# Optimization experiments

Hardware: AMD Instinct MI355X
Metric: run time of the kernel (lower is better)

The kernel has to match this reference:

```python
import jax, jax.numpy as jnp
import numpy as np

D_MODEL = 2048
D_STATE = 64
D_HEAD = 64
EXPAND = 2
CHUNK = 256
D_INNER = EXPAND * D_MODEL          # 4096
N_HEADS = D_INNER // D_HEAD          # 64
PARAM_DIM = 1 + 2 * D_STATE          # 129


def setup_inputs() -> dict:
    key = jax.random.key(0)
    k0, k1, k2, k3 = jax.random.split(key, 4)
    x = jax.random.normal(k0, (1, 4096, D_MODEL), jnp.float32)
    w_in = jax.random.normal(k1, (2 * D_INNER, D_MODEL), jnp.float32) * 0.02
    w_param = jax.random.normal(k2, (N_HEADS * PARAM_DIM, D_MODEL), jnp.float32) * 0.02
    w_out = jax.random.normal(k3, (D_MODEL, D_INNER), jnp.float32) * 0.02
    return {"x": x, "w_in": w_in, "w_param": w_param, "w_out": w_out}


def _ssd(a, Bm, Cm, X, Q):
    # a: (nb, l), Bm/Cm: (nb, l, ds), X: (nb, l, dh). Mamba-2 SSD chunked scan.
    nb, l = a.shape
    ds = Bm.shape[-1]
    dh = X.shape[-1]
    nc = l // Q
    la = jnp.log(a).reshape(nb, nc, Q)
    cs = jnp.cumsum(la, axis=-1)                      # cumulative log-decay within chunk
    Bc = Bm.reshape(nb, nc, Q, ds)
    Cc = Cm.reshape(nb, nc, Q, ds)
    Xc = X.reshape(nb, nc, Q, dh)
    # intra-chunk (attention-like dual): L[i,j] = prod_{r=j+1..i} a_r, j<=i
    tri = jnp.tril(jnp.ones((Q, Q), bool))
    L = jnp.where(tri, jnp.exp(cs[..., :, None] - cs[..., None, :]), 0.0)
    scores = jnp.einsum('znid,znjd->znij', Cc, Bc) * L
    y_diag = jnp.einsum('znij,znjh->znih', scores, Xc)
    # per-chunk state contribution: sum_j decay_to_end[j] * B_j^T x_j -> (nb,nc,ds,dh)
    decay_states = jnp.exp(cs[..., -1:] - cs)
    states = jnp.einsum('znj,znjd,znjh->zndh', decay_states, Bc, Xc)
    A_chunk = jnp.exp(cs[..., -1])                    # total decay per chunk (nb, nc)
    def step(S, inp):
        Ac, st = inp
        S_prev = S
        return Ac[:, None, None] * S + st, S_prev
    S0 = jnp.zeros((nb, ds, dh), a.dtype)
    _, S_prev = jax.lax.scan(step, S0, (A_chunk.T, jnp.moveaxis(states, 1, 0)))
    S_prev = jnp.moveaxis(S_prev, 0, 1)               # state entering each chunk (nb,nc,ds,dh)
    y_inter = jnp.einsum('znid,zndh,zni->znih', Cc, S_prev, jnp.exp(cs))
    return (y_diag + y_inter).reshape(nb, l, dh)


def reference(x, w_in, w_param, w_out):
    b, l, _ = x.shape
    xr = x @ w_in.T                                   # (b, l, 2*d_inner)
    inp, res = xr[..., :D_INNER], xr[..., D_INNER:]
    params = (x @ w_param.T).reshape(b, l, N_HEADS, PARAM_DIM)
    dt = jax.nn.softplus(params[..., 0])
    a = jnp.exp(-dt)                                  # (b, l, n_heads)
    Bp = params[..., 1:1 + D_STATE]
    Cp = params[..., 1 + D_STATE:]
    nb = b * N_HEADS
    # NOTE: raw row-major reshapes, mirroring the torch source exactly
    y = _ssd(a.reshape(nb, l),
             Bp.reshape(nb, l, D_STATE),
             Cp.reshape(nb, l, D_STATE),
             inp.reshape(nb, l, D_HEAD),
             CHUNK)
    y = y.reshape(b, l, D_INNER)
    out = y * jax.nn.silu(res)
    return out @ w_out.T
```

## Files before the change

### kernel.cpp

```cpp
#include <hip/hip_runtime.h>
#include <math.h>

#define Q 256

typedef unsigned short u16;
typedef unsigned int u32;
typedef __attribute__((ext_vector_type(8))) short short8;
typedef __attribute__((ext_vector_type(4))) float f32x4;

__device__ __forceinline__ float bf2f(u32 u){
  union { float f; u32 i; } v; v.i = u << 16; return v.f;
}
__device__ __forceinline__ u16 f2bf(float f){
  union { float f; u32 i; } v; v.f = f;
  u32 r = (v.i + 0x7FFFu + ((v.i >> 16) & 1u)) >> 16;
  return (u16)r;
}
__device__ __forceinline__ float softplusf(float x){
  return x > 20.f ? x : log1pf(expf(x));
}
__device__ __forceinline__ float siluf(float x){
  return x / (1.f + expf(-x));
}

__device__ __forceinline__ void gload_lds16(const void* g, const void* l){
  __builtin_amdgcn_global_load_lds(
    (const __attribute__((address_space(1))) void*)(uintptr_t)g,
    (__attribute__((address_space(3))) void*)(u32)(uintptr_t)l,
    16, 0, 0);
}

__device__ __forceinline__ u32 swz_off(int row, int col2){
  return (u32)(row*128 + (col2 ^ ((row & 7) << 4)));
}
__device__ __forceinline__ short8 frag_ld(const u16* buf, int row, int kk, int lk){
  return *(const short8*)((const char*)buf + row*128 + (((kk*4 + lk) ^ (row & 7)) << 4));
}

__global__ __launch_bounds__(256) void cast_bf16(const float* __restrict__ in,
    u16* __restrict__ out)
{
  const size_t i = ((size_t)blockIdx.x * 256 + threadIdx.x) * 4;
  const float4 v = *(const float4*)(in + i);
  ushort4 o;
  o.x = f2bf(v.x); o.y = f2bf(v.y); o.z = f2bf(v.z); o.w = f2bf(v.w);
  *(ushort4*)(out + i) = o;
}

#define G256_VM8 asm volatile("s_waitcnt vmcnt(8)" ::: "memory")
#define G256_VM4 asm volatile("s_waitcnt vmcnt(4)" ::: "memory")
#define G256_VM0 asm volatile("s_waitcnt vmcnt(0)" ::: "memory")

#define G256_STAGE(s_) \
  _Pragma("unroll") for (int q = 0; q < 4; q++) \
    gload_lds16(sptr[q] + (s_)*32, lds + (((s_)&3)*32768) + (q*512 + tid)*16);

#define G256_PHASE(p_, dostage_, VMSTMT) { \
  const char* sb_ = lds + (((p_)&3)*32768); \
  if (dostage_) { G256_STAGE((p_)+3) } \
  short8 af_[8], bf_[4]; \
  _Pragma("unroll") for (int m = 0; m < 8; m++) af_[m] = *(const short8*)(sb_ + aoff[m]); \
  _Pragma("unroll") for (int n = 0; n < 4; n++) bf_[n] = *(const short8*)(sb_ + boff[n]); \
  __builtin_amdgcn_s_setprio(1); \
  _Pragma("unroll") for (int m = 0; m < 8; m++) \
  _Pragma("unroll") for (int n = 0; n < 4; n++) \
    acc[m][n] = __builtin_amdgcn_mfma_f32_16x16x32_bf16(af_[m], bf_[n], acc[m][n], 0, 0, 0); \
  __builtin_amdgcn_s_setprio(0); \
  VMSTMT; \
  __builtin_amdgcn_s_barrier(); \
}

#define G256_CORE(A_, B_, K_, NTN_) \
  extern __shared__ char lds[]; \
  const int tid = threadIdx.x; \
  const int nwg = gridDim.x, bid = blockIdx.x; \
  const int wg = (bid & 7) * (nwg >> 3) + (bid >> 3); \
  const int m0 = (wg / (NTN_)) * 256, n0 = (wg % (NTN_)) * 256; \
  const int w = tid >> 6, l = tid & 63; \
  const int wr = w >> 2, wc = w & 3; \
  const int lr = l & 15, lk = l >> 4; \
  const u16* sptr[4]; \
  _Pragma("unroll") for (int q = 0; q < 4; q++) { \
    const int c = q*512 + tid; \
    const int r = c >> 3; \
    const int jl = (c & 7) ^ (r & 7); \
    sptr[q] = (jl < 4) ? ((A_) + (size_t)(m0 + r)*(K_) + jl*8) \
                       : ((B_) + (size_t)(n0 + r)*(K_) + (jl-4)*8); \
  } \
  int aoff[8], boff[4]; \
  _Pragma("unroll") for (int m = 0; m < 8; m++) { \
    const int r = wr*128 + m*16 + lr; \
    aoff[m] = r*128 + ((lk ^ (r & 7)) << 4); } \
  _Pragma("unroll") for (int n = 0; n < 4; n++) { \
    const int r = wc*64 + n*16 + lr; \
    boff[n] = r*128 + (((4 + lk) ^ (r & 7)) << 4); } \
  f32x4 acc[8][4]; \
  { f32x4 z = {0.f,0.f,0.f,0.f}; \
    _Pragma("unroll") for (int m = 0; m < 8; m++) \
    _Pragma("unroll") for (int n = 0; n < 4; n++) acc[m][n] = z; } \
  G256_STAGE(0) G256_STAGE(1) G256_STAGE(2) \
  G256_VM8; \
  __builtin_amdgcn_s_barrier(); \
  { const int NPH = (K_)/32; \
    for (int p = 0; p < NPH-4; p += 4) { \
      G256_PHASE(p,   1, G256_VM8) \
      G256_PHASE(p+1, 1, G256_VM8) \
      G256_PHASE(p+2, 1, G256_VM8) \
      G256_PHASE(p+3, 1, G256_VM8) \
    } \
    G256_PHASE(NPH-4, 1, G256_VM8) \
    G256_PHASE(NPH-3, 0, G256_VM4) \
    G256_PHASE(NPH-2, 0, G256_VM0) \
    G256_PHASE(NPH-1, 0, (void)0) \
  }

__global__ void __launch_bounds__(512, 2) gemm_in256(const u16* __restrict__ A,
    const u16* __restrict__ B, u16* __restrict__ inp, u16* __restrict__ resb)
{
  G256_CORE(A, B, 2048, 32)
  #pragma unroll
  for (int m = 0; m < 8; m++)
    #pragma unroll
    for (int n = 0; n < 4; n++) {
      const int col = n0 + wc*64 + n*16 + lr;
      #pragma unroll
      for (int j = 0; j < 4; j++) {
        const int row = m0 + wr*128 + m*16 + lk*4 + j;
        const u16 v = f2bf(acc[m][n][j]);
        if (col < 4096) inp[(size_t)row*4096 + col] = v;
        else            resb[(size_t)row*4096 + (col - 4096)] = v;
      }
    }
}

__global__ void __launch_bounds__(512, 2) gemm_par256(const u16* __restrict__ A,
    const u16* __restrict__ B, float* __restrict__ dtb,
    u16* __restrict__ Bb, u16* __restrict__ Cb)
{
  G256_CORE(A, B, 2048, 33)
  #pragma unroll
  for (int m = 0; m < 8; m++)
    #pragma unroll
    for (int n = 0; n < 4; n++) {
      const int col = n0 + wc*64 + n*16 + lr;
      if (col < 8256) {
        const int h = col / 129, rr = col - h*129;
        #pragma unroll
        for (int j = 0; j < 4; j++) {
          const int row = m0 + wr*128 + m*16 + lk*4 + j;
          const float v = acc[m][n][j];
          if (rr == 0)      dtb[(size_t)row*64 + h] = v;
          else if (rr < 65) Bb[((size_t)row*64 + h)*64 + (rr-1)]  = f2bf(v);
          else              Cb[((size_t)row*64 + h)*64 + (rr-65)] = f2bf(v);
        }
      }
    }
}

#define MFMA_GEMM_CORE(Abf_, Bbf_, K_) \
  __shared__ short As[128*64]; \
  __shared__ short Bs[128*64]; \
  const int tid = threadIdx.x; \
  const int w = tid >> 6, l = tid & 63; \
  const int m0 = blockIdx.y * 128, n0 = blockIdx.x * 128; \
  const int wr = (w >> 1) * 64, wc = (w & 1) * 64; \
  const int sub = l >> 3; \
  const int scol = ((l & 7) ^ sub) * 8; \
  const int lr16 = l & 15; \
  const int koff = (l >> 4) << 4; \
  const int swz = (l & 7) << 4; \
  f32x4 acc[4][4]; \
  { f32x4 z = {0.f, 0.f, 0.f, 0.f}; \
    _Pragma("unroll") for (int m_ = 0; m_ < 4; m_++) \
    _Pragma("unroll") for (int n_ = 0; n_ < 4; n_++) acc[m_][n_] = z; } \
  const u16* Agp = (Abf_) + (size_t)m0 * (K_); \
  const u16* Bgp = (Bbf_) + (size_t)n0 * (K_); \
  for (int kt = 0; kt < (K_); kt += 64) { \
    __syncthreads(); \
    _Pragma("unroll") for (int i_ = 0; i_ < 4; i_++) { \
      const int rbase = i_*32 + w*8; \
      gload_lds16(Agp + (size_t)(rbase + sub)*(K_) + kt + scol, As + rbase*64); \
      gload_lds16(Bgp + (size_t)(rbase + sub)*(K_) + kt + scol, Bs + rbase*64); \
    } \
    __syncthreads(); \
    short8 af[2][4], bf[2][4]; \
    _Pragma("unroll") for (int kk = 0; kk < 2; kk++) { \
      _Pragma("unroll") for (int m_ = 0; m_ < 4; m_++) \
        af[kk][m_] = *(const short8*)((const char*)As + (wr + m_*16 + lr16)*128 + ((kk*64 + koff) ^ swz)); \
      _Pragma("unroll") for (int n_ = 0; n_ < 4; n_++) \
        bf[kk][n_] = *(const short8*)((const char*)Bs + (wc + n_*16 + lr16)*128 + ((kk*64 + koff) ^ swz)); \
    } \
    _Pragma("unroll") for (int m_ = 0; m_ < 4; m_++) \
    _Pragma("unroll") for (int n_ = 0; n_ < 4; n_++) \
    _Pragma("unroll") for (int kk = 0; kk < 2; kk++) \
      acc[m_][n_] = __builtin_amdgcn_mfma_f32_16x16x32_bf16(af[kk][m_], bf[kk][n_], acc[m_][n_], 0, 0, 0); \
  } \
  const int orow0 = m0 + wr + ((l >> 4) << 2); \
  const int ocol0 = n0 + wc + (l & 15);

__global__ __launch_bounds__(256) void gemm_out(const u16* __restrict__ A,
    const u16* __restrict__ B, float* __restrict__ C)
{
  MFMA_GEMM_CORE(A, B, 4096)
  #pragma unroll
  for (int m_ = 0; m_ < 4; m_++)
    #pragma unroll
    for (int n_ = 0; n_ < 4; n_++) {
      const int col = ocol0 + n_*16;
      #pragma unroll
      for (int j = 0; j < 4; j++)
        C[(size_t)(orow0 + m_*16 + j)*2048 + col] = acc[m_][n_][j];
    }
}

__global__ __launch_bounds__(256) void ssd_phaseA(const float* __restrict__ dtb,
    const u16* __restrict__ Bb, const u16* __restrict__ inp,
    float* __restrict__ cs_g, float* __restrict__ achunk, float* __restrict__ states_t)
{
  const int g = blockIdx.x, tid = threadIdx.x;
  const int p = g * Q + tid;
  __shared__ float sc[Q];
  __shared__ u16 sBt[64*64];
  __shared__ u16 sXt[64*64];
  sc[tid] = -softplusf(dtb[p]);
  __syncthreads();
  for (int off = 1; off < Q; off <<= 1) {
    float v = (tid >= off) ? sc[tid - off] : 0.f;
    __syncthreads();
    if (tid >= off) sc[tid] += v;
    __syncthreads();
  }
  cs_g[p] = sc[tid];
  const float cl = sc[Q-1];
  if (tid == 0) achunk[g] = expf(cl);

  const int w = tid >> 6, l = tid & 63;
  const int lrow = l & 15, lk = l >> 4;
  const int tj = tid & 63, tcb = (tid >> 6) * 16;
  f32x4 acc[4];
  { f32x4 z = {0,0,0,0}; acc[0]=z; acc[1]=z; acc[2]=z; acc[3]=z; }

  for (int js = 0; js < 4; js++) {
    __syncthreads();
    {
      const int jc = js*64 + tj;
      const float wj = expf(cl - sc[jc]);
      const size_t prow = ((size_t)g*Q + jc) * 64;
      union { uint4 v; u16 s[8]; } b0, b1, x0, x1;
      b0.v = *(const uint4*)&Bb[prow + tcb];
      b1.v = *(const uint4*)&Bb[prow + tcb + 8];
      x0.v = *(const uint4*)&inp[prow + tcb];
      x1.v = *(const uint4*)&inp[prow + tcb + 8];
      #pragma unroll
      for (int q = 0; q < 8; q++) {
        const int r0 = tcb + q, r1 = tcb + 8 + q;
        *(u16*)((char*)sBt + swz_off(r0, 2*tj)) = f2bf(wj * bf2f((u32)b0.s[q]));
        *(u16*)((char*)sBt + swz_off(r1, 2*tj)) = f2bf(wj * bf2f((u32)b1.s[q]));
        *(u16*)((char*)sXt + swz_off(r0, 2*tj)) = x0.s[q];
        *(u16*)((char*)sXt + swz_off(r1, 2*tj)) = x1.s[q];
      }
    }
    __syncthreads();
    short8 aX0 = frag_ld(sXt, w*16 + lrow, 0, lk);
    short8 aX1 = frag_ld(sXt, w*16 + lrow, 1, lk);
    #pragma unroll
    for (int n = 0; n < 4; n++) {
      short8 b0 = frag_ld(sBt, n*16 + lrow, 0, lk);
      short8 b1 = frag_ld(sBt, n*16 + lrow, 1, lk);
      acc[n] = __builtin_amdgcn_mfma_f32_16x16x32_bf16(aX0, b0, acc[n], 0, 0, 0);
      acc[n] = __builtin_amdgcn_mfma_f32_16x16x32_bf16(aX1, b1, acc[n], 0, 0, 0);
    }
  }
  #pragma unroll
  for (int reg = 0; reg < 4; reg++) {
    const int d = w*16 + lk*4 + reg;
    #pragma unroll
    for (int n = 0; n < 4; n++)
      states_t[(size_t)g*4096 + d*64 + n*16 + lrow] = acc[n][reg];
  }
}

__global__ __launch_bounds__(256) void ssd_scan(float* __restrict__ states,
    const float* __restrict__ achunk)
{
  const int n = blockIdx.x, tid = threadIdx.x;
  float S[16];
  #pragma unroll
  for (int k = 0; k < 16; k++) S[k] = 0.f;
  for (int c = 0; c < 16; c++) {
    const int g = n*16 + c;
    const float A = achunk[g];
    #pragma unroll
    for (int k = 0; k < 16; k++) {
      const size_t e = (size_t)g * 4096 + tid + k*256;
      const float st = states[e];
      states[e] = S[k];
      S[k] = fmaf(A, S[k], st);
    }
  }
}

__global__ __launch_bounds__(256) void ssd_diag(const u16* __restrict__ Bb,
    const u16* __restrict__ Cb, const u16* __restrict__ inp,
    const float* __restrict__ cs_g, const float* __restrict__ states_t,
    const u16* __restrict__ resb, u16* __restrict__ yb)
{
  const int g = blockIdx.y, it = blockIdx.x, tid = threadIdx.x;
  const int w = tid >> 6, l = tid & 63;
  const int lrow = l & 15, lk = l >> 4;
  const int p_base = g * Q;
  __shared__ u16 sC[64*64];
  __shared__ u16 sB[64*64];
  __shared__ u16 sX[64*64];
  __shared__ u16 sP[64*64];
  __shared__ float csi[64], csj[64];

  const int r = tid >> 2, c0 = (tid & 3) << 4;
  {
    const size_t prow = (size_t)(p_base + it*64 + r) * 64;
    uint4 v0 = *(const uint4*)&Cb[prow + c0];
    uint4 v1 = *(const uint4*)&Cb[prow + c0 + 8];
    *(uint4*)((char*)sC + swz_off(r, c0*2))      = v0;
    *(uint4*)((char*)sC + swz_off(r, c0*2 + 16)) = v1;
    if (tid < 64) csi[tid] = cs_g[p_base + it*64 + tid];
  }
  const int i0 = w * 16;
  const int xj = tid & 63, xdb = (tid >> 6) * 16;
  f32x4 accY[4];
  { f32x4 z = {0,0,0,0}; accY[0]=z; accY[1]=z; accY[2]=z; accY[3]=z; }

  for (int jt = 0; jt <= it; jt++) {
    __syncthreads();
    {
      const size_t prow = (size_t)(p_base + jt*64 + r) * 64;
      uint4 v0 = *(const uint4*)&Bb[prow + c0];
      uint4 v1 = *(const uint4*)&Bb[prow + c0 + 8];
      *(uint4*)((char*)sB + swz_off(r, c0*2))      = v0;
      *(uint4*)((char*)sB + swz_off(r, c0*2 + 16)) = v1;
      if (tid < 64) csj[tid] = cs_g[p_base + jt*64 + tid];
    }
    {
      const size_t prow = (size_t)(p_base + jt*64 + xj) * 64;
      union { uint4 v; u16 s[8]; } x0, x1;
      x0.v = *(const uint4*)&inp[prow + xdb];
      x1.v = *(const uint4*)&inp[prow + xdb + 8];
      #pragma unroll
      for (int q = 0; q < 8; q++) {
        *(u16*)((char*)sX + swz_off(xdb + q,     2*xj)) = x0.s[q];
        *(u16*)((char*)sX + swz_off(xdb + 8 + q, 2*xj)) = x1.s[q];
      }
    }
    __syncthreads();
    f32x4 sAcc[4];
    { f32x4 z = {0,0,0,0}; sAcc[0]=z; sAcc[1]=z; sAcc[2]=z; sAcc[3]=z; }
    {
      short8 aC0 = frag_ld(sC, i0 + lrow, 0, lk);
      short8 aC1 = frag_ld(sC, i0 + lrow, 1, lk);
      #pragma unroll
      for (int n = 0; n < 4; n++) {
        short8 b0 = frag_ld(sB, n*16 + lrow, 0, lk);
        short8 b1 = frag_ld(sB, n*16 + lrow, 1, lk);
        sAcc[n] = __builtin_amdgcn_mfma_f32_16x16x32_bf16(aC0, b0, sAcc[n], 0, 0, 0);
        sAcc[n] = __builtin_amdgcn_mfma_f32_16x16x32_bf16(aC1, b1, sAcc[n], 0, 0, 0);
      }
    }
    const bool full = (jt < it);
    #pragma unroll
    for (int n = 0; n < 4; n++) {
      const int j_l = n*16 + lrow;
      const float cj = csj[j_l];
      #pragma unroll
      for (int reg = 0; reg < 4; reg++) {
        const int i_l = i0 + lk*4 + reg;
        float s = 0.f;
        if (full || j_l <= i_l) s = sAcc[n][reg] * expf(csi[i_l] - cj);
        *(u16*)((char*)sP + swz_off(i_l, n*32 + 2*lrow)) = f2bf(s);
      }
    }
    {
      short8 aP0 = frag_ld(sP, i0 + lrow, 0, lk);
      short8 aP1 = frag_ld(sP, i0 + lrow, 1, lk);
      #pragma unroll
      for (int n = 0; n < 4; n++) {
        short8 x0f = frag_ld(sX, n*16 + lrow, 0, lk);
        short8 x1f = frag_ld(sX, n*16 + lrow, 1, lk);
        accY[n] = __builtin_amdgcn_mfma_f32_16x16x32_bf16(aP0, x0f, accY[n], 0, 0, 0);
        accY[n] = __builtin_amdgcn_mfma_f32_16x16x32_bf16(aP1, x1f, accY[n], 0, 0, 0);
      }
    }
  }
  __syncthreads();
  {
    const int d = tid & 63, sb = (tid >> 6) * 16;
    const float* srow = &states_t[(size_t)g*4096 + d*64 + sb];
    float4 f0 = *(const float4*)(srow);
    float4 f1 = *(const float4*)(srow + 4);
    float4 f2 = *(const float4*)(srow + 8);
    float4 f3 = *(const float4*)(srow + 12);
    union { uint4 v; u16 s[8]; } o0, o1;
    o0.s[0]=f2bf(f0.x); o0.s[1]=f2bf(f0.y); o0.s[2]=f2bf(f0.z); o0.s[3]=f2bf(f0.w);
    o0.s[4]=f2bf(f1.x); o0.s[5]=f2bf(f1.y); o0.s[6]=f2bf(f1.z); o0.s[7]=f2bf(f1.w);
    o1.s[0]=f2bf(f2.x); o1.s[1]=f2bf(f2.y); o1.s[2]=f2bf(f2.z); o1.s[3]=f2bf(f2.w);
    o1.s[4]=f2bf(f3.x); o1.s[5]=f2bf(f3.y); o1.s[6]=f2bf(f3.z); o1.s[7]=f2bf(f3.w);
    *(uint4*)((char*)sB + swz_off(d, sb*2))      = o0.v;
    *(uint4*)((char*)sB + swz_off(d, sb*2 + 16)) = o1.v;
  }
  __syncthreads();
  f32x4 accI[4];
  { f32x4 z = {0,0,0,0}; accI[0]=z; accI[1]=z; accI[2]=z; accI[3]=z; }
  {
    short8 aC0 = frag_ld(sC, i0 + lrow, 0, lk);
    short8 aC1 = frag_ld(sC, i0 + lrow, 1, lk);
    #pragma unroll
    for (int n = 0; n < 4; n++) {
      short8 s0 = frag_ld(sB, n*16 + lrow, 0, lk);
      short8 s1 = frag_ld(sB, n*16 + lrow, 1, lk);
      accI[n] = __builtin_amdgcn_mfma_f32_16x16x32_bf16(aC0, s0, accI[n], 0, 0, 0);
      accI[n] = __builtin_amdgcn_mfma_f32_16x16x32_bf16(aC1, s1, accI[n], 0, 0, 0);
    }
  }
  #pragma unroll
  for (int reg = 0; reg < 4; reg++) {
    const int i_l = i0 + lk*4 + reg;
    const float ei = expf(csi[i_l]);
    const size_t prow = (size_t)(p_base + it*64 + i_l) * 64;
    #pragma unroll
    for (int n = 0; n < 4; n++) {
      const int d = n*16 + lrow;
      const float yv = accY[n][reg] + ei * accI[n][reg];
      const float rv = bf2f((u32)resb[prow + d]);
      yb[prow + d] = f2bf(yv * siluf(rv));
    }
  }
}

extern "C" void kernel_launch(void* const* d_in, const int* in_sizes, int n_in,
                              void* d_out, int out_size, void* d_ws, size_t ws_size,
                              hipStream_t stream)
{
  const float* x       = (const float*)d_in[0];
  const float* w_in    = (const float*)d_in[1];
  const float* w_param = (const float*)d_in[2];
  const float* w_out   = (const float*)d_in[3];
  float* out = (float*)d_out;
  char* ws = (char*)d_ws;

  float* states    = (float*)(ws);
  u16*   xb        = (u16*)  (ws);
  u16*   yb        = (u16*)  (ws + 0x1000000ull);
  u16*   w_in_b    = (u16*)  (ws + 0x1000000ull);
  u16*   w_param_b = (u16*)  (ws + 0x3000000ull);
  u16*   w_out_b   = (u16*)  (ws + 0x5100000ull);
  u16*   inp       = (u16*)  (ws + 0x6100000ull);
  u16*   resb      = (u16*)  (ws + 0x8100000ull);
  u16*   Bb        = (u16*)  (ws + 0xA100000ull);
  u16*   Cb        = (u16*)  (ws + 0xC100000ull);
  float* dtb       = (float*)(ws + 0xE100000ull);
  float* cs        = (float*)(ws + 0xE200000ull);
  float* achunk    = (float*)(ws + 0xE300000ull);

  hipFuncSetAttribute((const void*)gemm_in256,
      hipFuncAttributeMaxDynamicSharedMemorySize, 131072);
  hipFuncSetAttribute((const void*)gemm_par256,
      hipFuncAttributeMaxDynamicSharedMemorySize, 131072);

  cast_bf16<<<8192,  256, 0, stream>>>(x, xb);
  cast_bf16<<<16384, 256, 0, stream>>>(w_in, w_in_b);
  cast_bf16<<<16512, 256, 0, stream>>>(w_param, w_param_b);
  cast_bf16<<<8192,  256, 0, stream>>>(w_out, w_out_b);

  gemm_in256 <<<512, 512, 131072, stream>>>(xb, w_in_b, inp, resb);
  gemm_par256<<<528, 512, 131072, stream>>>(xb, w_param_b, dtb, Bb, Cb);
  ssd_phaseA<<<1024, 256, 0, stream>>>(dtb, Bb, inp, cs, achunk, states);
  ssd_scan<<<64, 256, 0, stream>>>(states, achunk);
  ssd_diag<<<dim3(4, 1024), 256, 0, stream>>>(Bb, Cb, inp, cs, states, resb, yb);
  gemm_out<<<dim3(16, 32), 256, 0, stream>>>(yb, w_out_b, out);
}
```

Baseline: 570.0 us.

## Double-buffer LDS fragment reads in 256x256 GEMM core to overlap with MFMA

Restructures the GEMM main loop so the LDS fragment reads for the next K-step are issued into a second register set while MFMAs run on the current one. The vmcnt waits are tightened and explicit lgkmcnt waits plus sched_barriers order the reads. Per-row swizzled offsets are replaced with a single base plus stride, relying on row&7 being constant across the m/n fragments. This is meant to hide LDS read latency behind matrix math, at the cost of more VGPRs, which may pressure the occupancy of 2 workgroups.

```diff
diff --git a/kernel.cpp b/kernel.cpp
--- a/kernel.cpp
+++ b/kernel.cpp
@@ -47,26 +47,38 @@
   *(ushort4*)(out + i) = o;
 }
 
-#define G256_VM8 asm volatile("s_waitcnt vmcnt(8)" ::: "memory")
 #define G256_VM4 asm volatile("s_waitcnt vmcnt(4)" ::: "memory")
 #define G256_VM0 asm volatile("s_waitcnt vmcnt(0)" ::: "memory")
+#define G256_LGKM12 asm volatile("s_waitcnt lgkmcnt(12)" ::: "memory"); \
+  __builtin_amdgcn_sched_barrier(0)
+#define G256_LGKM0 asm volatile("s_waitcnt lgkmcnt(0)" ::: "memory"); \
+  __builtin_amdgcn_sched_barrier(0)
 
 #define G256_STAGE(s_) \
   _Pragma("unroll") for (int q = 0; q < 4; q++) \
     gload_lds16(sptr[q] + (s_)*32, lds + (((s_)&3)*32768) + (q*512 + tid)*16);
 
-#define G256_PHASE(p_, dostage_, VMSTMT) { \
-  const char* sb_ = lds + (((p_)&3)*32768); \
-  if (dostage_) { G256_STAGE((p_)+3) } \
-  short8 af_[8], bf_[4]; \
-  _Pragma("unroll") for (int m = 0; m < 8; m++) af_[m] = *(const short8*)(sb_ + aoff[m]); \
-  _Pragma("unroll") for (int n = 0; n < 4; n++) bf_[n] = *(const short8*)(sb_ + boff[n]); \
+#define G256_READS(s_, AF, BF) { \
+  const char* sb_ = lds + (((s_)&3)*32768); \
+  _Pragma("unroll") for (int m = 0; m < 8; m++) \
+    AF[m] = *(const short8*)(sb_ + abase + m*2048); \
+  _Pragma("unroll") for (int n = 0; n < 4; n++) \
+    BF[n] = *(const short8*)(sb_ + bbase + n*2048); \
+}
+
+#define G256_MFMA(AF, BF) \
   __builtin_amdgcn_s_setprio(1); \
   _Pragma("unroll") for (int m = 0; m < 8; m++) \
   _Pragma("unroll") for (int n = 0; n < 4; n++) \
-    acc[m][n] = __builtin_amdgcn_mfma_f32_16x16x32_bf16(af_[m], bf_[n], acc[m][n], 0, 0, 0); \
-  __builtin_amdgcn_s_setprio(0); \
-  VMSTMT; \
+    acc[m][n] = __builtin_amdgcn_mfma_f32_16x16x32_bf16(AF[m], BF[n], acc[m][n], 0, 0, 0); \
+  __builtin_amdgcn_s_setprio(0);
+
+#define G256_PH(p_, CA, CB, NA, NB) { \
+  G256_READS((p_)+1, NA, NB) \
+  G256_STAGE((p_)+3) \
+  G256_LGKM12; \
+  G256_MFMA(CA, CB) \
+  G256_VM4; \
   __builtin_amdgcn_s_barrier(); \
 }
 
@@ -87,31 +99,39 @@
     sptr[q] = (jl < 4) ? ((A_) + (size_t)(m0 + r)*(K_) + jl*8) \
                        : ((B_) + (size_t)(n0 + r)*(K_) + (jl-4)*8); \
   } \
-  int aoff[8], boff[4]; \
-  _Pragma("unroll") for (int m = 0; m < 8; m++) { \
-    const int r = wr*128 + m*16 + lr; \
-    aoff[m] = r*128 + ((lk ^ (r & 7)) << 4); } \
-  _Pragma("unroll") for (int n = 0; n < 4; n++) { \
-    const int r = wc*64 + n*16 + lr; \
-    boff[n] = r*128 + (((4 + lk) ^ (r & 7)) << 4); } \
+  const int abase = (wr*128 + lr)*128 + ((lk ^ (lr & 7)) << 4); \
+  const int bbase = (wc*64  + lr)*128 + (((4 + lk) ^ (lr & 7)) << 4); \
   f32x4 acc[8][4]; \
   { f32x4 z = {0.f,0.f,0.f,0.f}; \
     _Pragma("unroll") for (int m = 0; m < 8; m++) \
     _Pragma("unroll") for (int n = 0; n < 4; n++) acc[m][n] = z; } \
+  short8 af0[8], bf0[4], af1[8], bf1[4]; \
   G256_STAGE(0) G256_STAGE(1) G256_STAGE(2) \
-  G256_VM8; \
+  G256_VM4; \
   __builtin_amdgcn_s_barrier(); \
+  G256_READS(0, af0, bf0) \
   { const int NPH = (K_)/32; \
     for (int p = 0; p < NPH-4; p += 4) { \
-      G256_PHASE(p,   1, G256_VM8) \
-      G256_PHASE(p+1, 1, G256_VM8) \
-      G256_PHASE(p+2, 1, G256_VM8) \
-      G256_PHASE(p+3, 1, G256_VM8) \
+      G256_PH(p,   af0, bf0, af1, bf1) \
+      G256_PH(p+1, af1, bf1, af0, bf0) \
+      G256_PH(p+2, af0, bf0, af1, bf1) \
+      G256_PH(p+3, af1, bf1, af0, bf0) \
     } \
-    G256_PHASE(NPH-4, 1, G256_VM8) \
-    G256_PHASE(NPH-3, 0, G256_VM4) \
-    G256_PHASE(NPH-2, 0, G256_VM0) \
-    G256_PHASE(NPH-1, 0, (void)0) \
+    G256_PH(NPH-4, af0, bf0, af1, bf1) \
+     \
+    { G256_READS(NPH-2, af0, bf0) \
+      G256_LGKM12; \
+      G256_MFMA(af1, bf1) \
+      G256_VM0; \
+      __builtin_amdgcn_s_barrier(); } \
+     \
+    { G256_READS(NPH-1, af1, bf1) \
+      G256_LGKM12; \
+      G256_MFMA(af0, bf0) \
+      __builtin_amdgcn_s_barrier(); } \
+     \
+    { G256_LGKM0; \
+      G256_MFMA(af1, bf1) } \
   }
 
 __global__ void __launch_bounds__(512, 2) gemm_in256(const u16* __restrict__ A,
```

Measured after the change: 697.1 us. +22.3%, slower.

## Restructure 256x256 GEMM pipeline to double-buffered K=64 stages

Applied to the files above, without the earlier changes.

Replaces the 4-deep, K=32-per-stage LDS ring buffer in the shared 256x256 GEMM core with a 2-deep buffer that loads K=64 per stage. Each iteration issues 32 MFMAs per wave and waits on vmcnt(0) before the barrier. This halves the number of barriers and waits per K, and each phase does more MFMA work. In exchange, only one stage is in flight ahead of compute, so latency hiding is shallower. With occupancy 2 and 128KB of LDS per block, LDS pressure also changes.

```diff
diff --git a/kernel.cpp b/kernel.cpp
--- a/kernel.cpp
+++ b/kernel.cpp
@@ -47,28 +47,27 @@
   *(ushort4*)(out + i) = o;
 }
 
-#define G256_VM8 asm volatile("s_waitcnt vmcnt(8)" ::: "memory")
-#define G256_VM4 asm volatile("s_waitcnt vmcnt(4)" ::: "memory")
 #define G256_VM0 asm volatile("s_waitcnt vmcnt(0)" ::: "memory")
 
 #define G256_STAGE(s_) \
-  _Pragma("unroll") for (int q = 0; q < 4; q++) \
-    gload_lds16(sptr[q] + (s_)*32, lds + (((s_)&3)*32768) + (q*512 + tid)*16);
-
-#define G256_PHASE(p_, dostage_, VMSTMT) { \
-  const char* sb_ = lds + (((p_)&3)*32768); \
-  if (dostage_) { G256_STAGE((p_)+3) } \
-  short8 af_[8], bf_[4]; \
-  _Pragma("unroll") for (int m = 0; m < 8; m++) af_[m] = *(const short8*)(sb_ + aoff[m]); \
-  _Pragma("unroll") for (int n = 0; n < 4; n++) bf_[n] = *(const short8*)(sb_ + boff[n]); \
+  _Pragma("unroll") for (int q = 0; q < 8; q++) \
+    gload_lds16(sptr[q] + (size_t)(s_)*64, lds + (((s_)&1)*65536) + (q*512 + tid)*16);
+
+#define G256_READS(sb_, AF, BF) \
+  _Pragma("unroll") for (int kk = 0; kk < 2; kk++) { \
+    _Pragma("unroll") for (int m = 0; m < 8; m++) \
+      AF[kk][m] = *(const short8*)((sb_) + abase[kk] + m*4096); \
+    _Pragma("unroll") for (int n = 0; n < 4; n++) \
+      BF[kk][n] = *(const short8*)((sb_) + bbase[kk] + n*4096); \
+  }
+
+#define G256_MFMA(AF, BF) \
   __builtin_amdgcn_s_setprio(1); \
   _Pragma("unroll") for (int m = 0; m < 8; m++) \
   _Pragma("unroll") for (int n = 0; n < 4; n++) \
-    acc[m][n] = __builtin_amdgcn_mfma_f32_16x16x32_bf16(af_[m], bf_[n], acc[m][n], 0, 0, 0); \
-  __builtin_amdgcn_s_setprio(0); \
-  VMSTMT; \
-  __builtin_amdgcn_s_barrier(); \
-}
+  _Pragma("unroll") for (int kk = 0; kk < 2; kk++) \
+    acc[m][n] = __builtin_amdgcn_mfma_f32_16x16x32_bf16(AF[kk][m], BF[kk][n], acc[m][n], 0, 0, 0); \
+  __builtin_amdgcn_s_setprio(0);
 
 #define G256_CORE(A_, B_, K_, NTN_) \
   extern __shared__ char lds[]; \
@@ -79,39 +78,41 @@
   const int w = tid >> 6, l = tid & 63; \
   const int wr = w >> 2, wc = w & 3; \
   const int lr = l & 15, lk = l >> 4; \
-  const u16* sptr[4]; \
-  _Pragma("unroll") for (int q = 0; q < 4; q++) { \
+  const u16* sptr[8]; \
+  _Pragma("unroll") for (int q = 0; q < 8; q++) { \
     const int c = q*512 + tid; \
-    const int r = c >> 3; \
-    const int jl = (c & 7) ^ (r & 7); \
-    sptr[q] = (jl < 4) ? ((A_) + (size_t)(m0 + r)*(K_) + jl*8) \
-                       : ((B_) + (size_t)(n0 + r)*(K_) + (jl-4)*8); \
+    const int r = c >> 4; \
+    const int jc = c & 15; \
+    const int jl = (jc & 7) ^ (r & 7); \
+    sptr[q] = (jc < 8) ? ((A_) + (size_t)(m0 + r)*(K_) + jl*8) \
+                       : ((B_) + (size_t)(n0 + r)*(K_) + jl*8); \
   } \
-  int aoff[8], boff[4]; \
-  _Pragma("unroll") for (int m = 0; m < 8; m++) { \
-    const int r = wr*128 + m*16 + lr; \
-    aoff[m] = r*128 + ((lk ^ (r & 7)) << 4); } \
-  _Pragma("unroll") for (int n = 0; n < 4; n++) { \
-    const int r = wc*64 + n*16 + lr; \
-    boff[n] = r*128 + (((4 + lk) ^ (r & 7)) << 4); } \
+  int abase[2], bbase[2]; \
+  _Pragma("unroll") for (int kk = 0; kk < 2; kk++) { \
+    abase[kk] = (wr*128 + lr)*256 + (((kk*4 + lk) ^ (lr & 7)) << 4); \
+    bbase[kk] = (wc*64  + lr)*256 + ((8 + ((kk*4 + lk) ^ (lr & 7))) << 4); \
+  } \
   f32x4 acc[8][4]; \
   { f32x4 z = {0.f,0.f,0.f,0.f}; \
     _Pragma("unroll") for (int m = 0; m < 8; m++) \
     _Pragma("unroll") for (int n = 0; n < 4; n++) acc[m][n] = z; } \
-  G256_STAGE(0) G256_STAGE(1) G256_STAGE(2) \
-  G256_VM8; \
+  G256_STAGE(0) \
+  G256_VM0; \
   __builtin_amdgcn_s_barrier(); \
-  { const int NPH = (K_)/32; \
-    for (int p = 0; p < NPH-4; p += 4) { \
-      G256_PHASE(p,   1, G256_VM8) \
-      G256_PHASE(p+1, 1, G256_VM8) \
-      G256_PHASE(p+2, 1, G256_VM8) \
-      G256_PHASE(p+3, 1, G256_VM8) \
+  { const int NPH = (K_)/64; \
+    for (int p = 0; p < NPH-1; ++p) { \
+      const char* sb_ = lds + ((p & 1)*65536); \
+      short8 af_[2][8], bf_[2][4]; \
+      G256_STAGE(p+1) \
+      G256_READS(sb_, af_, bf_) \
+      G256_MFMA(af_, bf_) \
+      G256_VM0; \
+      __builtin_amdgcn_s_barrier(); \
     } \
-    G256_PHASE(NPH-4, 1, G256_VM8) \
-    G256_PHASE(NPH-3, 0, G256_VM4) \
-    G256_PHASE(NPH-2, 0, G256_VM0) \
-    G256_PHASE(NPH-1, 0, (void)0) \
+    { const char* sb_ = lds + (((NPH-1) & 1)*65536); \
+      short8 af_[2][8], bf_[2][4]; \
+      G256_READS(sb_, af_, bf_) \
+      G256_MFMA(af_, bf_) } \
   }
 
 __global__ void __launch_bounds__(512, 2) gemm_in256(const u16* __restrict__ A,
```

New measurement: 570.0 us. No clear change (-0.0%).
